# Kernel optimization log

Hardware: AMD Instinct MI355X
Metric: run time of the kernel (lower is better)

The kernel has to match this reference:

```python
import jax, jax.numpy as jnp
import numpy as np

DIM = 1024
STATE = 64
HEADS = 8
EXPAND = 2
INNER = DIM * EXPAND          # 2048
HEAD_DIM = INNER // HEADS     # 256
KERNEL = 4
B, L = 2, 2048
EPS = 1e-5


def setup_inputs() -> dict:
    key = jax.random.key(0)
    ks = jax.random.split(key, 12)
    s = 0.02
    return {
        "input_tensor": jax.random.normal(ks[0], (B, L, DIM), jnp.float32),
        "Wx": jax.random.normal(ks[1], (INNER, DIM), jnp.float32) * s,
        "Wz": jax.random.normal(ks[2], (INNER, DIM), jnp.float32) * s,
        "conv_w": jax.random.normal(ks[3], (INNER, 1, KERNEL), jnp.float32) * s,
        "conv_b": jnp.zeros((INNER,), jnp.float32),
        "Wb": jax.random.normal(ks[4], (HEADS * STATE, INNER), jnp.float32) * s,
        "Wc": jax.random.normal(ks[5], (HEADS * STATE, INNER), jnp.float32) * s,
        "Wdt": jax.random.normal(ks[6], (HEADS, INNER), jnp.float32) * s,
        "b_dt": jnp.zeros((HEADS,), jnp.float32),
        "log_a": jnp.log(jnp.full((HEADS,), 0.5, jnp.float32)),
        "d_param": jnp.ones((HEADS,), jnp.float32),
        "gn_w": jnp.ones((INNER,), jnp.float32),
        "gn_b": jnp.zeros((INNER,), jnp.float32),
        "Wout": jax.random.normal(ks[7], (DIM, INNER), jnp.float32) * s,
    }


def _causal_conv(x, conv_w, conv_b):
    # x: (B, L, INNER); depthwise conv, kernel 4, left-pad 3 (causal)
    x_pad = jnp.pad(x, ((0, 0), (KERNEL - 1, 0), (0, 0)))
    w = conv_w[:, 0, :]  # (INNER, K)
    y = sum(x_pad[:, k:k + x.shape[1], :] * w[:, k] for k in range(KERNEL))
    return y + conv_b


def _ssd_scan(x, b, c, dt, a):
    # x: (B,L,H,P) b,c: (B,L,H,N) dt: (B,L,H) a: (H,)
    state0 = jnp.zeros((x.shape[0], HEADS, STATE, HEAD_DIM), x.dtype)

    def step(state, inp):
        x_t, b_t, c_t, dt_t = inp  # (B,H,P),(B,H,N),(B,H,N),(B,H)
        decay = jnp.exp(dt_t * a)[..., None, None]          # (B,H,1,1)
        b_bar = (dt_t[..., None] * b_t)                      # (B,H,N)
        state = decay * state + b_bar[..., None] * x_t[:, :, None, :]
        y_t = jnp.einsum("bhn,bhnp->bhp", c_t, state)
        return state, y_t

    xs = (x.transpose(1, 0, 2, 3), b.transpose(1, 0, 2, 3),
          c.transpose(1, 0, 2, 3), dt.transpose(1, 0, 2))
    _, ys = jax.lax.scan(step, state0, xs)  # ys: (L,B,H,P)
    return ys.transpose(1, 0, 2, 3)


def reference(input_tensor, Wx, Wz, conv_w, conv_b, Wb, Wc, Wdt, b_dt,
              log_a, d_param, gn_w, gn_b, Wout):
    bsz, seq, _ = input_tensor.shape
    x = input_tensor @ Wx.T               # (B,L,INNER)
    z = input_tensor @ Wz.T
    x = _causal_conv(x, conv_w, conv_b)
    x = jax.nn.silu(x)
    b = (x @ Wb.T).reshape(bsz, seq, HEADS, STATE)
    c = (x @ Wc.T).reshape(bsz, seq, HEADS, STATE)
    dt = jax.nn.softplus(x @ Wdt.T + b_dt)  # (B,L,H)
    xh = x.reshape(bsz, seq, HEADS, HEAD_DIM)
    a = -jnp.exp(log_a)
    y = _ssd_scan(xh, b, c, dt, a)
    y = y + d_param[None, None, :, None] * xh
    # GroupNorm(HEADS, INNER) applied on (B, C, L): normalize per (batch, group)
    # over (channels-in-group, sequence)
    yg = y  # (B, L, H, P) -- groups are contiguous channel blocks = heads
    mean = yg.mean(axis=(1, 3), keepdims=True)
    var = yg.var(axis=(1, 3), keepdims=True)
    yn = (yg - mean) / jnp.sqrt(var + EPS)
    yn = yn * gn_w.reshape(1, 1, HEADS, HEAD_DIM) + gn_b.reshape(1, 1, HEADS, HEAD_DIM)
    yn = yn.reshape(bsz, seq, INNER)
    out = yn * jax.nn.silu(z)
    return out @ Wout.T
```

## Files before the change

### kernel.cpp

```cpp
#include <hip/hip_runtime.h>
#include <math.h>

#define DIM_   1024
#define STATE_ 64
#define HEADS_ 8
#define INNER_ 2048
#define HDIM_  256
#define B_     2
#define L_     2048
#define M_     (B_*L_)
#define EPS_   1e-5f
#define Q_     64
#define NC_    (L_/Q_)
#define NCHUNK_ (B_*HEADS_*NC_)
#define BCS_   1024
#define XZS_   4096

typedef _Float16 f16;
typedef __attribute__((ext_vector_type(8))) _Float16 half8;
typedef __attribute__((ext_vector_type(4))) _Float16 half4;
typedef __attribute__((ext_vector_type(4))) float    f32x4;

__device__ __forceinline__ float siluf(float x) { return x / (1.f + expf(-x)); }

__device__ __forceinline__ void gload_lds16(const void* g, void* l) {
    __builtin_amdgcn_global_load_lds((const __attribute__((address_space(1))) void*)g,
                                     (__attribute__((address_space(3))) void*)l, 16, 0, 0);
}

__global__ __launch_bounds__(256) void cast_all(const float* __restrict__ in0,
                                                const float* __restrict__ Wx,
                                                const float* __restrict__ Wz,
                                                const float* __restrict__ Wb,
                                                const float* __restrict__ Wc,
                                                const float* __restrict__ Wout,
                                                f16* __restrict__ input_h,
                                                f16* __restrict__ wxz_h,
                                                f16* __restrict__ wbc_h,
                                                f16* __restrict__ wout_h) {
    int i = blockIdx.x * 256 + threadIdx.x;
    const float* src; f16* dst; int off;
    if      (i < 1048576) { src = in0;  dst = input_h;            off = i; }
    else if (i < 1572864) { src = Wx;   dst = wxz_h;              off = i - 1048576; }
    else if (i < 2097152) { src = Wz;   dst = wxz_h + 2097152;    off = i - 1572864; }
    else if (i < 2359296) { src = Wb;   dst = wbc_h;              off = i - 2097152; }
    else if (i < 2621440) { src = Wc;   dst = wbc_h + 1048576;    off = i - 2359296; }
    else                  { src = Wout; dst = wout_h;             off = i - 2621440; }
    float4 v = *(const float4*)&src[(size_t)off * 4];
    half4 o;
    o[0] = (f16)v.x; o[1] = (f16)v.y; o[2] = (f16)v.z; o[3] = (f16)v.w;
    *(half4*)&dst[(size_t)off * 4] = o;
}

template<int BN, bool OUTF16>
__global__ __launch_bounds__(256) void hgemm(const f16* __restrict__ A,
                                             const f16* __restrict__ W,
                                             void* __restrict__ Cout,
                                             int K, int N) {
    constexpr int N_FR = BN / 32;
    constexpr int NITER = (128 + BN) / 64;
    __shared__ f16 sA[128 * 32];
    __shared__ f16 sW[BN * 32];
    const int tid  = threadIdx.x;
    const int wid  = tid >> 6;
    const int lane = tid & 63;
    const int bm = blockIdx.y * 128;
    const int bn = blockIdx.x * BN;
    const int wr = wid >> 1, wc = wid & 1;
    const int r  = lane & 15, kg = lane >> 4;

    const f16* gsrc[NITER];
    f16* ldst[NITER];
#pragma unroll
    for (int i = 0; i < NITER; ++i) {
        int slot = tid + i * 256;
        if (slot < 512) {
            int row = slot >> 2;
            int kgv = ((slot & 3) ^ ((row >> 1) & 3)) * 8;
            gsrc[i] = A + (size_t)(bm + row) * K + kgv;
        } else {
            int row = (slot - 512) >> 2;
            int kgv = ((slot & 3) ^ ((row >> 1) & 3)) * 8;
            gsrc[i] = W + (size_t)(bn + row) * K + kgv;
        }
        int slot0 = (tid & ~63) + i * 256;
        ldst[i] = (slot0 < 512) ? &sA[slot0 * 8] : &sW[(slot0 - 512) * 8];
    }

    int aoff[4], boff[N_FR];
#pragma unroll
    for (int m = 0; m < 4; ++m) {
        int arow = wr * 64 + m * 16 + r;
        aoff[m] = arow * 32 + ((kg ^ ((arow >> 1) & 3)) << 3);
    }
#pragma unroll
    for (int n = 0; n < N_FR; ++n) {
        int wrow = wc * (BN / 2) + n * 16 + r;
        boff[n] = wrow * 32 + ((kg ^ ((wrow >> 1) & 3)) << 3);
    }

    f32x4 acc[4][N_FR];
#pragma unroll
    for (int m = 0; m < 4; ++m)
#pragma unroll
        for (int n = 0; n < N_FR; ++n) acc[m][n] = (f32x4)0.f;

    for (int k0 = 0; k0 < K; k0 += 32) {
#pragma unroll
        for (int i = 0; i < NITER; ++i) gload_lds16(gsrc[i] + k0, ldst[i]);
        __syncthreads();
        half8 av[4], bv[N_FR];
#pragma unroll
        for (int m = 0; m < 4; ++m) av[m] = *(const half8*)&sA[aoff[m]];
#pragma unroll
        for (int n = 0; n < N_FR; ++n) bv[n] = *(const half8*)&sW[boff[n]];
#pragma unroll
        for (int m = 0; m < 4; ++m)
#pragma unroll
            for (int n = 0; n < N_FR; ++n)
                acc[m][n] = __builtin_amdgcn_mfma_f32_16x16x32_f16(av[m], bv[n], acc[m][n], 0, 0, 0);
        __syncthreads();
    }

#pragma unroll
    for (int m = 0; m < 4; ++m)
#pragma unroll
        for (int n = 0; n < N_FR; ++n) {
            int row0o = bm + wr * 64 + m * 16 + kg * 4;
            int col   = bn + wc * (BN / 2) + n * 16 + r;
#pragma unroll
            for (int j = 0; j < 4; ++j) {
                if (OUTF16) ((f16*)Cout)[(size_t)(row0o + j) * N + col] = (f16)acc[m][n][j];
                else        ((float*)Cout)[(size_t)(row0o + j) * N + col] = acc[m][n][j];
            }
        }
}

__global__ __launch_bounds__(256) void conv_silu_dt(const f16* __restrict__ xz,
                                                    const float* __restrict__ cw,
                                                    const float* __restrict__ cb,
                                                    const float* __restrict__ Wdt,
                                                    const float* __restrict__ bdt,
                                                    f16* __restrict__ xc,
                                                    float* __restrict__ dtb) {
    __shared__ float sred[4][HEADS_];
    const int m = blockIdx.x;
    const int tid = threadIdx.x;
    const int c8 = tid * 8;
    const int t = m & (L_ - 1);
    float acc[8];
    float4 wv[8];
#pragma unroll
    for (int j = 0; j < 8; ++j) { acc[j] = cb[c8 + j]; wv[j] = *(const float4*)&cw[(c8 + j) * 4]; }
#pragma unroll
    for (int k = 0; k < 4; ++k) {
        int tt = t - 3 + k;
        if (tt >= 0) {
            half8 xv = *(const half8*)&xz[(size_t)(m - 3 + k) * XZS_ + c8];
#pragma unroll
            for (int j = 0; j < 8; ++j) acc[j] += (float)xv[j] * ((const float*)&wv[j])[k];
        }
    }
    float xf[8];
    half8 o;
#pragma unroll
    for (int j = 0; j < 8; ++j) { xf[j] = siluf(acc[j]); o[j] = (f16)xf[j]; }
    *(half8*)&xc[(size_t)m * INNER_ + c8] = o;

    float p[HEADS_];
#pragma unroll
    for (int h = 0; h < HEADS_; ++h) {
        float4 w0 = *(const float4*)&Wdt[h * INNER_ + c8];
        float4 w1 = *(const float4*)&Wdt[h * INNER_ + c8 + 4];
        p[h] = xf[0]*w0.x + xf[1]*w0.y + xf[2]*w0.z + xf[3]*w0.w
             + xf[4]*w1.x + xf[5]*w1.y + xf[6]*w1.z + xf[7]*w1.w;
    }
#pragma unroll
    for (int h = 0; h < HEADS_; ++h)
#pragma unroll
        for (int off = 32; off > 0; off >>= 1)
            p[h] += __shfl_down(p[h], off, 64);
    if ((tid & 63) == 0) {
#pragma unroll
        for (int h = 0; h < HEADS_; ++h) sred[tid >> 6][h] = p[h];
    }
    __syncthreads();
    if (tid < 32) {
        float v = sred[tid >> 3][tid & 7];
        v += __shfl_down(v, 16, 32);
        v += __shfl_down(v, 8, 32);
        if (tid < 8) {
            float s = v + bdt[tid];
            dtb[(size_t)m * HEADS_ + tid] = (s > 20.f) ? s : log1pf(expf(s));
        }
    }
}

__global__ __launch_bounds__(256) void xpose_k(const f16* __restrict__ xc,
                                               f16* __restrict__ xT) {
    __shared__ f16 sT[64][72];
    const int blk = blockIdx.x;
    const int bh = blk >> 7;
    const int rem = blk & 127;
    const int tt = rem >> 2;
    const int pt = rem & 3;
    const int b = bh >> 3, h = bh & 7;
    const int tid = threadIdx.x;
#pragma unroll
    for (int it = 0; it < 2; ++it) {
        int q = tid + it * 256;
        int tr = q >> 3;
        int p0 = (q & 7) * 8;
        half8 v = *(const half8*)&xc[(size_t)(b * L_ + tt * 64 + tr) * INNER_ + h * HDIM_ + pt * 64 + p0];
        *(half8*)&sT[tr][p0] = v;
    }
    __syncthreads();
#pragma unroll
    for (int it = 0; it < 2; ++it) {
        int q = tid + it * 256;
        int pr = q >> 3;
        int t0 = (q & 7) * 8;
        half8 v;
#pragma unroll
        for (int j = 0; j < 8; ++j) v[j] = sT[t0 + j][pr];
        *(half8*)&xT[((size_t)bh * HDIM_ + pt * 64 + pr) * L_ + tt * 64 + t0] = v;
    }
}

__global__ __launch_bounds__(256) void ssd_phase1(const f16* __restrict__ bc,
                                                  const float* __restrict__ dtb,
                                                  const float* __restrict__ log_a,
                                                  f16* __restrict__ pbuf,
                                                  float* __restrict__ eAbuf,
                                                  float* __restrict__ wbuf,
                                                  float* __restrict__ cdecay) {
    __shared__ float sA[Q_];
    __shared__ float sDt[Q_];
    const int tid = threadIdx.x;
    const int chunk = blockIdx.x;
    const int bh = chunk / NC_;
    const int ck = chunk - bh * NC_;
    const int b = bh >> 3, h = bh & 7;
    const int m0 = b * L_ + ck * Q_;

    if (tid < 64) {
        float dt = dtb[(size_t)(m0 + tid) * HEADS_ + h];
        float a = -expf(log_a[h]);
        float x = dt * a;
#pragma unroll
        for (int off = 1; off < 64; off <<= 1) {
            float v = __shfl_up(x, off, 64);
            if (tid >= off) x += v;
        }
        float Alast = __shfl(x, 63, 64);
        sA[tid] = x;
        sDt[tid] = dt;
        eAbuf[(size_t)(m0 + tid) * HEADS_ + h] = expf(x);
        wbuf[(size_t)chunk * Q_ + tid] = expf(Alast - x) * dt;
        if (tid == 0) cdecay[chunk] = expf(Alast);
    }
    __syncthreads();

    const int w = tid >> 6, lane = tid & 63;
    const int r = lane & 15, kg = lane >> 4;
    const int ft = w;
    const f16* Crow = bc + (size_t)(m0 + ft * 16 + r) * BCS_ + 512 + h * STATE_;
    half8 a0 = *(const half8*)(Crow + kg * 8);
    half8 a1 = *(const half8*)(Crow + 32 + kg * 8);
#pragma unroll
    for (int fs = 0; fs < 4; ++fs) {
        const f16* Brow = bc + (size_t)(m0 + fs * 16 + r) * BCS_ + h * STATE_;
        half8 b0 = *(const half8*)(Brow + kg * 8);
        half8 b1 = *(const half8*)(Brow + 32 + kg * 8);
        f32x4 g = (f32x4)0.f;
        g = __builtin_amdgcn_mfma_f32_16x16x32_f16(a0, b0, g, 0, 0, 0);
        g = __builtin_amdgcn_mfma_f32_16x16x32_f16(a1, b1, g, 0, 0, 0);
        int s = fs * 16 + r;
        float As = sA[s], dts = sDt[s];
#pragma unroll
        for (int j = 0; j < 4; ++j) {
            int t = ft * 16 + kg * 4 + j;
            float val = (t >= s) ? g[j] * expf(sA[t] - As) * dts : 0.f;
            pbuf[((size_t)chunk * Q_ + t) * Q_ + s] = (f16)val;
        }
    }
}

__global__ __launch_bounds__(256) void bwt_k(const f16* __restrict__ bc,
                                             const float* __restrict__ wbuf,
                                             f16* __restrict__ bwT) {
    __shared__ f16 sT[64][72];
    __shared__ float sw[64];
    const int chunk = blockIdx.x;
    const int bh = chunk / NC_;
    const int ck = chunk - bh * NC_;
    const int b = bh >> 3, h = bh & 7;
    const int m0 = b * L_ + ck * Q_;
    const int tid = threadIdx.x;
    if (tid < 64) sw[tid] = wbuf[(size_t)chunk * Q_ + tid];
#pragma unroll
    for (int it = 0; it < 2; ++it) {
        int q = tid + it * 256;
        int s = q >> 3;
        int n0 = (q & 7) * 8;
        half8 v = *(const half8*)&bc[(size_t)(m0 + s) * BCS_ + h * STATE_ + n0];
        *(half8*)&sT[s][n0] = v;
    }
    __syncthreads();
#pragma unroll
    for (int it = 0; it < 2; ++it) {
        int q = tid + it * 256;
        int n = q >> 3;
        int s0 = (q & 7) * 8;
        half8 o;
#pragma unroll
        for (int j = 0; j < 8; ++j) o[j] = (f16)((float)sT[s0 + j][n] * sw[s0 + j]);
        *(half8*)&bwT[((size_t)chunk * Q_ + n) * Q_ + s0] = o;
    }
}

__global__ __launch_bounds__(256) void ssd_phase2(const f16* __restrict__ xT,
                                                  const f16* __restrict__ bwT,
                                                  f16* __restrict__ sloc) {
    const int tid = threadIdx.x;
    const int chunk = blockIdx.x;
    const int bh = chunk / NC_;
    const int ck = chunk - bh * NC_;
    const int w = tid >> 6, lane = tid & 63;
    const int r = lane & 15, kg = lane >> 4;

    f32x4 acc[4][4];
#pragma unroll
    for (int i = 0; i < 4; ++i)
#pragma unroll
        for (int j = 0; j < 4; ++j) acc[i][j] = (f32x4)0.f;

#pragma unroll
    for (int kk = 0; kk < 2; ++kk) {
        half8 a[4], bfr[4];
#pragma unroll
        for (int pf = 0; pf < 4; ++pf) {
            int p = w * 64 + pf * 16 + r;
            a[pf] = *(const half8*)&xT[((size_t)bh * HDIM_ + p) * L_ + ck * Q_ + kk * 32 + kg * 8];
        }
#pragma unroll
        for (int nf = 0; nf < 4; ++nf) {
            int n = nf * 16 + r;
            bfr[nf] = *(const half8*)&bwT[((size_t)chunk * Q_ + n) * Q_ + kk * 32 + kg * 8];
        }
#pragma unroll
        for (int pf = 0; pf < 4; ++pf)
#pragma unroll
            for (int nf = 0; nf < 4; ++nf)
                acc[pf][nf] = __builtin_amdgcn_mfma_f32_16x16x32_f16(a[pf], bfr[nf], acc[pf][nf], 0, 0, 0);
    }
#pragma unroll
    for (int pf = 0; pf < 4; ++pf)
#pragma unroll
        for (int nf = 0; nf < 4; ++nf) {
            int n = nf * 16 + r;
#pragma unroll
            for (int j = 0; j < 4; ++j) {
                int p = w * 64 + pf * 16 + kg * 4 + j;
                sloc[((size_t)chunk * HDIM_ + p) * STATE_ + n] = (f16)acc[pf][nf][j];
            }
        }
}

__global__ __launch_bounds__(256) void chunk_scan_k(f16* __restrict__ sloc,
                                                    const float* __restrict__ cdecay) {
    int bh = blockIdx.x >> 6;
    int el = (blockIdx.x & 63) * 256 + threadIdx.x;
    float s = 0.f;
    for (int c = 0; c < NC_; ++c) {
        size_t chunk = (size_t)bh * NC_ + c;
        f16* ptr = sloc + chunk * (size_t)(STATE_*HDIM_) + el;
        float tmp = (float)*ptr;
        *ptr = (f16)s;
        s = cdecay[chunk] * s + tmp;
    }
}

__global__ __launch_bounds__(256) void ssd_phase3(const f16* __restrict__ bc,
                                                  const f16* __restrict__ pbuf,
                                                  const f16* __restrict__ xT,
                                                  const f16* __restrict__ sloc,
                                                  const f16* __restrict__ xch,
                                                  const float* __restrict__ eAbuf,
                                                  const float* __restrict__ dparam,
                                                  f16* __restrict__ ybuf,
                                                  float* __restrict__ gstats) {
    __shared__ float red[512];
    const int tid = threadIdx.x;
    const int chunk = blockIdx.x;
    const int bh = chunk / NC_;
    const int ck = chunk - bh * NC_;
    const int b = bh >> 3, h = bh & 7;
    const int m0 = b * L_ + ck * Q_;
    const int w = tid >> 6, lane = tid & 63;
    const int r = lane & 15, kg = lane >> 4;

    float eA[4];
#pragma unroll
    for (int ft = 0; ft < 4; ++ft)
        eA[ft] = eAbuf[(size_t)(m0 + ft * 16 + r) * HEADS_ + h];

    f32x4 acc[4][4];
#pragma unroll
    for (int i = 0; i < 4; ++i)
#pragma unroll
        for (int j = 0; j < 4; ++j) acc[i][j] = (f32x4)0.f;

#pragma unroll
    for (int ks = 0; ks < 4; ++ks) {
        half8 a[4], bfr[4];
#pragma unroll
        for (int ft = 0; ft < 4; ++ft) {
            int t = ft * 16 + r;
            if (ks < 2) {
                a[ft] = *(const half8*)&pbuf[((size_t)chunk * Q_ + t) * Q_ + ks * 32 + kg * 8];
            } else {
                half8 c = *(const half8*)&bc[(size_t)(m0 + t) * BCS_ + 512 + h * STATE_ + (ks - 2) * 32 + kg * 8];
                half8 sc;
#pragma unroll
                for (int j = 0; j < 8; ++j) sc[j] = (f16)(eA[ft] * (float)c[j]);
                a[ft] = sc;
            }
        }
#pragma unroll
        for (int pf = 0; pf < 4; ++pf) {
            int p = w * 64 + pf * 16 + r;
            if (ks < 2)
                bfr[pf] = *(const half8*)&xT[((size_t)bh * HDIM_ + p) * L_ + ck * Q_ + ks * 32 + kg * 8];
            else
                bfr[pf] = *(const half8*)&sloc[((size_t)chunk * HDIM_ + p) * STATE_ + (ks - 2) * 32 + kg * 8];
        }
#pragma unroll
        for (int ft = 0; ft < 4; ++ft)
#pragma unroll
            for (int pf = 0; pf < 4; ++pf)
                acc[ft][pf] = __builtin_amdgcn_mfma_f32_16x16x32_f16(a[ft], bfr[pf], acc[ft][pf], 0, 0, 0);
    }

    const float d = dparam[h];
    float lsum = 0.f, lsq = 0.f;
#pragma unroll
    for (int ft = 0; ft < 4; ++ft)
#pragma unroll
        for (int pf = 0; pf < 4; ++pf) {
            int p = w * 64 + pf * 16 + r;
#pragma unroll
            for (int j = 0; j < 4; ++j) {
                int t = ft * 16 + kg * 4 + j;
                size_t off = (size_t)(m0 + t) * INNER_ + h * HDIM_ + p;
                float y = acc[ft][pf][j] + d * (float)xch[off];
                ybuf[off] = (f16)y;
                lsum += y; lsq += y * y;
            }
        }
    __syncthreads();
    red[tid] = lsum; red[256 + tid] = lsq;
    __syncthreads();
    for (int st = 128; st > 0; st >>= 1) {
        if (tid < st) { red[tid] += red[tid + st]; red[256 + tid] += red[256 + tid + st]; }
        __syncthreads();
    }
    if (tid == 0) {
        atomicAdd(&gstats[bh * 2 + 0], red[0]);
        atomicAdd(&gstats[bh * 2 + 1], red[256]);
    }
}

__global__ __launch_bounds__(256) void gn_gate_h(const f16* __restrict__ ybuf,
                                                 const f16* __restrict__ xz,
                                                 const float* __restrict__ gstats,
                                                 const float* __restrict__ gnw,
                                                 const float* __restrict__ gnb,
                                                 f16* __restrict__ g) {
    int idx = blockIdx.x * 256 + threadIdx.x;
    int c8 = (idx & (INNER_/8 - 1)) * 8;
    int m = idx >> 8;
    int bh = (m >> 11) * HEADS_ + (c8 >> 8);
    const float cnt = (float)(L_ * HDIM_);
    float mean = gstats[bh*2] / cnt;
    float var  = gstats[bh*2+1] / cnt - mean*mean;
    float rstd = rsqrtf(var + EPS_);
    size_t off = (size_t)m * INNER_ + c8;
    half8 yv = *(const half8*)&ybuf[off];
    half8 zv = *(const half8*)&xz[(size_t)m * XZS_ + INNER_ + c8];
    float4 w0 = *(const float4*)&gnw[c8], w1 = *(const float4*)&gnw[c8+4];
    float4 b0 = *(const float4*)&gnb[c8], b1 = *(const float4*)&gnb[c8+4];
    float wv[8] = {w0.x, w0.y, w0.z, w0.w, w1.x, w1.y, w1.z, w1.w};
    float bv[8] = {b0.x, b0.y, b0.z, b0.w, b1.x, b1.y, b1.z, b1.w};
    half8 o;
#pragma unroll
    for (int j = 0; j < 8; ++j) {
        float v = ((float)yv[j] - mean) * rstd * wv[j] + bv[j];
        o[j] = (f16)(v * siluf((float)zv[j]));
    }
    *(half8*)&g[off] = o;
}

extern "C" void kernel_launch(void* const* d_in, const int* in_sizes, int n_in,
                              void* d_out, int out_size, void* d_ws, size_t ws_size,
                              hipStream_t stream) {
    const float* input  = (const float*)d_in[0];
    const float* Wx     = (const float*)d_in[1];
    const float* Wz     = (const float*)d_in[2];
    const float* conv_w = (const float*)d_in[3];
    const float* conv_b = (const float*)d_in[4];
    const float* Wb     = (const float*)d_in[5];
    const float* Wc     = (const float*)d_in[6];
    const float* Wdt    = (const float*)d_in[7];
    const float* b_dt   = (const float*)d_in[8];
    const float* log_a  = (const float*)d_in[9];
    const float* d_par  = (const float*)d_in[10];
    const float* gn_w   = (const float*)d_in[11];
    const float* gn_b   = (const float*)d_in[12];
    const float* Wout   = (const float*)d_in[13];
    float* out = (float*)d_out;

    float* ws = (float*)d_ws;
    size_t off = 0;
    auto alloc = [&](size_t nfloats) { float* p = ws + off; off += (nfloats + 63) & ~(size_t)63; return p; };
    f16* input_h = (f16*)alloc((size_t)M_*DIM_/2);
    f16* wxz_h   = (f16*)alloc((size_t)XZS_*DIM_/2);
    f16* wbc_h   = (f16*)alloc((size_t)BCS_*INNER_/2);
    f16* wout_h  = (f16*)alloc((size_t)DIM_*INNER_/2);
    f16* xz_h    = (f16*)alloc((size_t)M_*XZS_/2);
    f16* xconv_h = (f16*)alloc((size_t)M_*INNER_/2);
    f16* xT_h    = (f16*)alloc((size_t)M_*INNER_/2);
    f16* gbuf_h  = (f16*)alloc((size_t)M_*INNER_/2);
    f16* bcmat_h = (f16*)alloc((size_t)M_*BCS_/2);
    f16* pbuf_h  = (f16*)alloc((size_t)NCHUNK_*Q_*Q_/2);
    f16* bwT_h   = (f16*)alloc((size_t)NCHUNK_*Q_*Q_/2);
    f16* sloc_h  = (f16*)alloc((size_t)NCHUNK_*STATE_*HDIM_/2);
    f16* ybuf_h  = (f16*)alloc((size_t)M_*INNER_/2);
    float* dtb   = alloc((size_t)M_*HEADS_);
    float* eAb   = alloc((size_t)M_*HEADS_);
    float* wbuf  = alloc((size_t)NCHUNK_*Q_);
    float* cdec  = alloc((size_t)NCHUNK_);
    float* gstat = alloc((size_t)2*B_*HEADS_);

    dim3 blk(256);

    cast_all<<<12288, blk, 0, stream>>>(input, Wx, Wz, Wb, Wc, Wout,
                                        input_h, wxz_h, wbc_h, wout_h);
    hgemm<128,true><<<dim3(XZS_/128, M_/128), blk, 0, stream>>>(input_h, wxz_h, xz_h, DIM_, XZS_);
    conv_silu_dt<<<M_, blk, 0, stream>>>(xz_h, conv_w, conv_b, Wdt, b_dt, xconv_h, dtb);
    hgemm<64,true><<<dim3(BCS_/64, M_/128), blk, 0, stream>>>(xconv_h, wbc_h, bcmat_h, INNER_, BCS_);
    xpose_k<<<2048, blk, 0, stream>>>(xconv_h, xT_h);
    ssd_phase1<<<NCHUNK_, blk, 0, stream>>>(bcmat_h, dtb, log_a, pbuf_h, eAb, wbuf, cdec);
    bwt_k<<<NCHUNK_, blk, 0, stream>>>(bcmat_h, wbuf, bwT_h);
    ssd_phase2<<<NCHUNK_, blk, 0, stream>>>(xT_h, bwT_h, sloc_h);
    chunk_scan_k<<<B_*HEADS_*64, blk, 0, stream>>>(sloc_h, cdec);
    hipMemsetAsync(gstat, 0, 2*B_*HEADS_*sizeof(float), stream);
    ssd_phase3<<<NCHUNK_, blk, 0, stream>>>(bcmat_h, pbuf_h, xT_h, sloc_h, xconv_h,
                                            eAb, d_par, ybuf_h, gstat);
    gn_gate_h<<<(M_*(INNER_/8))/256, blk, 0, stream>>>(ybuf_h, xz_h, gstat, gn_w, gn_b, gbuf_h);
    hgemm<64,false><<<dim3(DIM_/64, M_/128), blk, 0, stream>>>(gbuf_h, wout_h, out, INNER_, DIM_);
}
```

Before: 363.3 us.

## Fuse SSD phases, groupnorm-gate into out GEMM, silu into xz GEMM

Merges ssd_phase1, bwt_k and ssd_phase2 into one kernel that keeps the dt-weighted B matrix in swizzled LDS instead of round-tripping through global memory. Applies silu to z in the xz GEMM epilogue and folds the groupnorm+gate into the A-tile load of the output GEMM, which removes the gbuf intermediate. It also vectorises chunk_scan to 4 elements per thread and replaces the memset by zeroing inside xpose_k. The cost is redundant normalisation work per N-tile in the output GEMM, plus fp16-cast gn weights and a fused A path that is not async.

```diff
diff --git a/kernel.cpp b/kernel.cpp
--- a/kernel.cpp
+++ b/kernel.cpp
@@ -34,10 +34,14 @@
                                                 const float* __restrict__ Wb,
                                                 const float* __restrict__ Wc,
                                                 const float* __restrict__ Wout,
+                                                const float* __restrict__ gw,
+                                                const float* __restrict__ gb,
                                                 f16* __restrict__ input_h,
                                                 f16* __restrict__ wxz_h,
                                                 f16* __restrict__ wbc_h,
-                                                f16* __restrict__ wout_h) {
+                                                f16* __restrict__ wout_h,
+                                                f16* __restrict__ gnw_h,
+                                                f16* __restrict__ gnb_h) {
     int i = blockIdx.x * 256 + threadIdx.x;
     const float* src; f16* dst; int off;
     if      (i < 1048576) { src = in0;  dst = input_h;            off = i; }
@@ -45,14 +49,16 @@
     else if (i < 2097152) { src = Wz;   dst = wxz_h + 2097152;    off = i - 1572864; }
     else if (i < 2359296) { src = Wb;   dst = wbc_h;              off = i - 2097152; }
     else if (i < 2621440) { src = Wc;   dst = wbc_h + 1048576;    off = i - 2359296; }
-    else                  { src = Wout; dst = wout_h;             off = i - 2621440; }
+    else if (i < 3145728) { src = Wout; dst = wout_h;             off = i - 2621440; }
+    else if (i < 3146240) { src = gw;   dst = gnw_h;              off = i - 3145728; }
+    else                  { src = gb;   dst = gnb_h;              off = i - 3146240; }
     float4 v = *(const float4*)&src[(size_t)off * 4];
     half4 o;
     o[0] = (f16)v.x; o[1] = (f16)v.y; o[2] = (f16)v.z; o[3] = (f16)v.w;
     *(half4*)&dst[(size_t)off * 4] = o;
 }
 
-template<int BN, bool OUTF16>
+template<int BN, bool OUTF16, bool SILUZ>
 __global__ __launch_bounds__(256) void hgemm(const f16* __restrict__ A,
                                              const f16* __restrict__ W,
                                              void* __restrict__ Cout,
@@ -130,8 +136,10 @@
             int col   = bn + wc * (BN / 2) + n * 16 + r;
 #pragma unroll
             for (int j = 0; j < 4; ++j) {
-                if (OUTF16) ((f16*)Cout)[(size_t)(row0o + j) * N + col] = (f16)acc[m][n][j];
-                else        ((float*)Cout)[(size_t)(row0o + j) * N + col] = acc[m][n][j];
+                float v = acc[m][n][j];
+                if (SILUZ && col >= INNER_) v = siluf(v);
+                if (OUTF16) ((f16*)Cout)[(size_t)(row0o + j) * N + col] = (f16)v;
+                else        ((float*)Cout)[(size_t)(row0o + j) * N + col] = v;
             }
         }
 }
@@ -197,7 +205,8 @@
 }
 
 __global__ __launch_bounds__(256) void xpose_k(const f16* __restrict__ xc,
-                                               f16* __restrict__ xT) {
+                                               f16* __restrict__ xT,
+                                               float* __restrict__ gstat) {
     __shared__ f16 sT[64][72];
     const int blk = blockIdx.x;
     const int bh = blk >> 7;
@@ -206,6 +215,7 @@
     const int pt = rem & 3;
     const int b = bh >> 3, h = bh & 7;
     const int tid = threadIdx.x;
+    if (blk == 0 && tid < 2 * B_ * HEADS_) gstat[tid] = 0.f;
 #pragma unroll
     for (int it = 0; it < 2; ++it) {
         int q = tid + it * 256;
@@ -227,15 +237,16 @@
     }
 }
 
-__global__ __launch_bounds__(256) void ssd_phase1(const f16* __restrict__ bc,
-                                                  const float* __restrict__ dtb,
-                                                  const float* __restrict__ log_a,
-                                                  f16* __restrict__ pbuf,
-                                                  float* __restrict__ eAbuf,
-                                                  float* __restrict__ wbuf,
-                                                  float* __restrict__ cdecay) {
-    __shared__ float sA[Q_];
-    __shared__ float sDt[Q_];
+__global__ __launch_bounds__(256) void ssd12(const f16* __restrict__ bc,
+                                             const float* __restrict__ dtb,
+                                             const float* __restrict__ log_a,
+                                             const f16* __restrict__ xT,
+                                             f16* __restrict__ pbuf,
+                                             f16* __restrict__ sloc,
+                                             float* __restrict__ eAbuf,
+                                             float* __restrict__ cdecay) {
+    __shared__ float sA[Q_], sDt[Q_], sw[Q_];
+    __shared__ f16 sB[Q_ * Q_];
     const int tid = threadIdx.x;
     const int chunk = blockIdx.x;
     const int bh = chunk / NC_;
@@ -243,6 +254,11 @@
     const int b = bh >> 3, h = bh & 7;
     const int m0 = b * L_ + ck * Q_;
 
+    const int s0 = tid >> 3,        n00 = (tid & 7) * 8;
+    const int s1 = (tid + 256) >> 3, n01 = (tid & 7) * 8;
+    half8 bv0 = *(const half8*)&bc[(size_t)(m0 + s0) * BCS_ + h * STATE_ + n00];
+    half8 bv1 = *(const half8*)&bc[(size_t)(m0 + s1) * BCS_ + h * STATE_ + n01];
+
     if (tid < 64) {
         float dt = dtb[(size_t)(m0 + tid) * HEADS_ + h];
         float a = -expf(log_a[h]);
@@ -255,79 +271,48 @@
         float Alast = __shfl(x, 63, 64);
         sA[tid] = x;
         sDt[tid] = dt;
+        sw[tid] = expf(Alast - x) * dt;
         eAbuf[(size_t)(m0 + tid) * HEADS_ + h] = expf(x);
-        wbuf[(size_t)chunk * Q_ + tid] = expf(Alast - x) * dt;
         if (tid == 0) cdecay[chunk] = expf(Alast);
     }
     __syncthreads();
+
+    {
+        float w0 = sw[s0], w1 = sw[s1];
+        half8 o0, o1;
+#pragma unroll
+        for (int j = 0; j < 8; ++j) { o0[j] = (f16)((float)bv0[j] * w0); o1[j] = (f16)((float)bv1[j] * w1); }
+        *(half8*)&sB[s0 * Q_ + (n00 ^ ((s0 & 7) << 3))] = o0;
+        *(half8*)&sB[s1 * Q_ + (n01 ^ ((s1 & 7) << 3))] = o1;
+    }
 
     const int w = tid >> 6, lane = tid & 63;
     const int r = lane & 15, kg = lane >> 4;
-    const int ft = w;
-    const f16* Crow = bc + (size_t)(m0 + ft * 16 + r) * BCS_ + 512 + h * STATE_;
-    half8 a0 = *(const half8*)(Crow + kg * 8);
-    half8 a1 = *(const half8*)(Crow + 32 + kg * 8);
-#pragma unroll
-    for (int fs = 0; fs < 4; ++fs) {
-        const f16* Brow = bc + (size_t)(m0 + fs * 16 + r) * BCS_ + h * STATE_;
-        half8 b0 = *(const half8*)(Brow + kg * 8);
-        half8 b1 = *(const half8*)(Brow + 32 + kg * 8);
-        f32x4 g = (f32x4)0.f;
-        g = __builtin_amdgcn_mfma_f32_16x16x32_f16(a0, b0, g, 0, 0, 0);
-        g = __builtin_amdgcn_mfma_f32_16x16x32_f16(a1, b1, g, 0, 0, 0);
-        int s = fs * 16 + r;
-        float As = sA[s], dts = sDt[s];
-#pragma unroll
-        for (int j = 0; j < 4; ++j) {
-            int t = ft * 16 + kg * 4 + j;
-            float val = (t >= s) ? g[j] * expf(sA[t] - As) * dts : 0.f;
-            pbuf[((size_t)chunk * Q_ + t) * Q_ + s] = (f16)val;
-        }
-    }
-}
-
-__global__ __launch_bounds__(256) void bwt_k(const f16* __restrict__ bc,
-                                             const float* __restrict__ wbuf,
-                                             f16* __restrict__ bwT) {
-    __shared__ f16 sT[64][72];
-    __shared__ float sw[64];
-    const int chunk = blockIdx.x;
-    const int bh = chunk / NC_;
-    const int ck = chunk - bh * NC_;
-    const int b = bh >> 3, h = bh & 7;
-    const int m0 = b * L_ + ck * Q_;
-    const int tid = threadIdx.x;
-    if (tid < 64) sw[tid] = wbuf[(size_t)chunk * Q_ + tid];
-#pragma unroll
-    for (int it = 0; it < 2; ++it) {
-        int q = tid + it * 256;
-        int s = q >> 3;
-        int n0 = (q & 7) * 8;
-        half8 v = *(const half8*)&bc[(size_t)(m0 + s) * BCS_ + h * STATE_ + n0];
-        *(half8*)&sT[s][n0] = v;
+
+    {
+        const int ft = w;
+        const f16* Crow = bc + (size_t)(m0 + ft * 16 + r) * BCS_ + 512 + h * STATE_;
+        half8 a0 = *(const half8*)(Crow + kg * 8);
+        half8 a1 = *(const half8*)(Crow + 32 + kg * 8);
+#pragma unroll
+        for (int fs = 0; fs < 4; ++fs) {
+            const f16* Brow = bc + (size_t)(m0 + fs * 16 + r) * BCS_ + h * STATE_;
+            half8 b0 = *(const half8*)(Brow + kg * 8);
+            half8 b1 = *(const half8*)(Brow + 32 + kg * 8);
+            f32x4 g = (f32x4)0.f;
+            g = __builtin_amdgcn_mfma_f32_16x16x32_f16(a0, b0, g, 0, 0, 0);
+            g = __builtin_amdgcn_mfma_f32_16x16x32_f16(a1, b1, g, 0, 0, 0);
+            int s = fs * 16 + r;
+            float As = sA[s], dts = sDt[s];
+#pragma unroll
+            for (int j = 0; j < 4; ++j) {
+                int t = ft * 16 + kg * 4 + j;
+                float val = (t >= s) ? g[j] * expf(sA[t] - As) * dts : 0.f;
+                pbuf[((size_t)chunk * Q_ + t) * Q_ + s] = (f16)val;
+            }
+        }
     }
     __syncthreads();
-#pragma unroll
-    for (int it = 0; it < 2; ++it) {
-        int q = tid + it * 256;
-        int n = q >> 3;
-        int s0 = (q & 7) * 8;
-        half8 o;
-#pragma unroll
-        for (int j = 0; j < 8; ++j) o[j] = (f16)((float)sT[s0 + j][n] * sw[s0 + j]);
-        *(half8*)&bwT[((size_t)chunk * Q_ + n) * Q_ + s0] = o;
-    }
-}
-
-__global__ __launch_bounds__(256) void ssd_phase2(const f16* __restrict__ xT,
-                                                  const f16* __restrict__ bwT,
-                                                  f16* __restrict__ sloc) {
-    const int tid = threadIdx.x;
-    const int chunk = blockIdx.x;
-    const int bh = chunk / NC_;
-    const int ck = chunk - bh * NC_;
-    const int w = tid >> 6, lane = tid & 63;
-    const int r = lane & 15, kg = lane >> 4;
 
     f32x4 acc[4][4];
 #pragma unroll
@@ -346,7 +331,13 @@
 #pragma unroll
         for (int nf = 0; nf < 4; ++nf) {
             int n = nf * 16 + r;
-            bfr[nf] = *(const half8*)&bwT[((size_t)chunk * Q_ + n) * Q_ + kk * 32 + kg * 8];
+            half8 v;
+#pragma unroll
+            for (int j = 0; j < 8; ++j) {
+                int s = kk * 32 + kg * 8 + j;
+                v[j] = sB[s * Q_ + (n ^ (j << 3))];
+            }
+            bfr[nf] = v;
         }
 #pragma unroll
         for (int pf = 0; pf < 4; ++pf)
@@ -369,15 +360,20 @@
 
 __global__ __launch_bounds__(256) void chunk_scan_k(f16* __restrict__ sloc,
                                                     const float* __restrict__ cdecay) {
-    int bh = blockIdx.x >> 6;
-    int el = (blockIdx.x & 63) * 256 + threadIdx.x;
-    float s = 0.f;
+    int bh = blockIdx.x >> 4;
+    int el4 = (((blockIdx.x & 15) * 256 + threadIdx.x) << 2);
+    float s0 = 0.f, s1 = 0.f, s2 = 0.f, s3 = 0.f;
     for (int c = 0; c < NC_; ++c) {
         size_t chunk = (size_t)bh * NC_ + c;
-        f16* ptr = sloc + chunk * (size_t)(STATE_*HDIM_) + el;
-        float tmp = (float)*ptr;
-        *ptr = (f16)s;
-        s = cdecay[chunk] * s + tmp;
+        f16* ptr = sloc + chunk * (size_t)(STATE_ * HDIM_) + el4;
+        half4 v = *(const half4*)ptr;
+        half4 o; o[0] = (f16)s0; o[1] = (f16)s1; o[2] = (f16)s2; o[3] = (f16)s3;
+        *(half4*)ptr = o;
+        float d = cdecay[chunk];
+        s0 = d * s0 + (float)v[0];
+        s1 = d * s1 + (float)v[1];
+        s2 = d * s2 + (float)v[2];
+        s3 = d * s3 + (float)v[3];
     }
 }
 
@@ -471,34 +467,115 @@
     }
 }
 
-__global__ __launch_bounds__(256) void gn_gate_h(const f16* __restrict__ ybuf,
-                                                 const f16* __restrict__ xz,
-                                                 const float* __restrict__ gstats,
-                                                 const float* __restrict__ gnw,
-                                                 const float* __restrict__ gnb,
-                                                 f16* __restrict__ g) {
-    int idx = blockIdx.x * 256 + threadIdx.x;
-    int c8 = (idx & (INNER_/8 - 1)) * 8;
-    int m = idx >> 8;
-    int bh = (m >> 11) * HEADS_ + (c8 >> 8);
-    const float cnt = (float)(L_ * HDIM_);
-    float mean = gstats[bh*2] / cnt;
-    float var  = gstats[bh*2+1] / cnt - mean*mean;
-    float rstd = rsqrtf(var + EPS_);
-    size_t off = (size_t)m * INNER_ + c8;
-    half8 yv = *(const half8*)&ybuf[off];
-    half8 zv = *(const half8*)&xz[(size_t)m * XZS_ + INNER_ + c8];
-    float4 w0 = *(const float4*)&gnw[c8], w1 = *(const float4*)&gnw[c8+4];
-    float4 b0 = *(const float4*)&gnb[c8], b1 = *(const float4*)&gnb[c8+4];
-    float wv[8] = {w0.x, w0.y, w0.z, w0.w, w1.x, w1.y, w1.z, w1.w};
-    float bv[8] = {b0.x, b0.y, b0.z, b0.w, b1.x, b1.y, b1.z, b1.w};
-    half8 o;
-#pragma unroll
-    for (int j = 0; j < 8; ++j) {
-        float v = ((float)yv[j] - mean) * rstd * wv[j] + bv[j];
-        o[j] = (f16)(v * siluf((float)zv[j]));
-    }
-    *(half8*)&g[off] = o;
+__global__ __launch_bounds__(256) void hgemm_gate(const f16* __restrict__ ybuf,
+                                                  const f16* __restrict__ xz,
+                                                  const f16* __restrict__ W,
+                                                  const float* __restrict__ gstats,
+                                                  const f16* __restrict__ gnw,
+                                                  const f16* __restrict__ gnb,
+                                                  float* __restrict__ Cout) {
+    constexpr int BN = 64;
+    const int K = INNER_, N = DIM_;
+    __shared__ f16 sA[128 * 32];
+    __shared__ f16 sW[BN * 32];
+    const int tid  = threadIdx.x;
+    const int wid  = tid >> 6;
+    const int lane = tid & 63;
+    const int bm = blockIdx.y * 128;
+    const int bn = blockIdx.x * BN;
+    const int wr = wid >> 1, wc = wid & 1;
+    const int r  = lane & 15, kg = lane >> 4;
+    const float INV_CNT = 1.f / ((float)L_ * HDIM_);
+
+    const int wrow = tid >> 2;
+    const int wkgv = (((tid + 512) & 3) ^ ((wrow >> 1) & 3)) * 8;
+    const f16* gW = W + (size_t)(bn + wrow >= 0 ? bn + wrow : 0) * K + wkgv;
+    f16* lW = &sW[(tid & ~63) * 8];
+
+    int aoff[4], boff[2];
+#pragma unroll
+    for (int m = 0; m < 4; ++m) {
+        int arow = wr * 64 + m * 16 + r;
+        aoff[m] = arow * 32 + ((kg ^ ((arow >> 1) & 3)) << 3);
+    }
+#pragma unroll
+    for (int n = 0; n < 2; ++n) {
+        int wrw = wc * 32 + n * 16 + r;
+        boff[n] = wrw * 32 + ((kg ^ ((wrw >> 1) & 3)) << 3);
+    }
+
+    int srow[2], skgv[2], sm[2];
+#pragma unroll
+    for (int i = 0; i < 2; ++i) {
+        int slot = tid + i * 256;
+        srow[i] = slot >> 2;
+        skgv[i] = ((slot & 3) ^ ((srow[i] >> 1) & 3)) * 8;
+        sm[i] = bm + srow[i];
+    }
+
+    half8 pyv[2], psz[2], pgw[2], pgb[2];
+    auto loadA = [&](int k0) {
+#pragma unroll
+        for (int i = 0; i < 2; ++i) {
+            int c = k0 + skgv[i];
+            pyv[i] = *(const half8*)&ybuf[(size_t)sm[i] * INNER_ + c];
+            psz[i] = *(const half8*)&xz[(size_t)sm[i] * XZS_ + INNER_ + c];
+            pgw[i] = *(const half8*)&gnw[c];
+            pgb[i] = *(const half8*)&gnb[c];
+        }
+    };
+    loadA(0);
+
+    f32x4 acc[4][2];
+#pragma unroll
+    for (int m = 0; m < 4; ++m)
+#pragma unroll
+        for (int n = 0; n < 2; ++n) acc[m][n] = (f32x4)0.f;
+
+    for (int k0 = 0; k0 < K; k0 += 32) {
+        gload_lds16(gW + k0, lW);
+#pragma unroll
+        for (int i = 0; i < 2; ++i) {
+            int c = k0 + skgv[i];
+            int bhid = ((sm[i] >> 11) << 3) + (c >> 8);
+            float mean = gstats[bhid * 2] * INV_CNT;
+            float var  = gstats[bhid * 2 + 1] * INV_CNT - mean * mean;
+            float rstd = rsqrtf(var + EPS_);
+            half8 o;
+#pragma unroll
+            for (int j = 0; j < 8; ++j) {
+                float Aj = rstd * (float)pgw[i][j];
+                float Cj = (float)pgb[i][j] - mean * Aj;
+                float v  = (float)pyv[i][j] * Aj + Cj;
+                o[j] = (f16)(v * (float)psz[i][j]);
+            }
+            *(half8*)&sA[(tid + i * 256) * 8] = o;
+        }
+        if (k0 + 32 < K) loadA(k0 + 32);
+        __syncthreads();
+        half8 av[4], bv[2];
+#pragma unroll
+        for (int m = 0; m < 4; ++m) av[m] = *(const half8*)&sA[aoff[m]];
+#pragma unroll
+        for (int n = 0; n < 2; ++n) bv[n] = *(const half8*)&sW[boff[n]];
+#pragma unroll
+        for (int m = 0; m < 4; ++m)
+#pragma unroll
+            for (int n = 0; n < 2; ++n)
+                acc[m][n] = __builtin_amdgcn_mfma_f32_16x16x32_f16(av[m], bv[n], acc[m][n], 0, 0, 0);
+        __syncthreads();
+    }
+
+#pragma unroll
+    for (int m = 0; m < 4; ++m)
+#pragma unroll
+        for (int n = 0; n < 2; ++n) {
+            int row0o = bm + wr * 64 + m * 16 + kg * 4;
+            int col   = bn + wc * 32 + n * 16 + r;
+#pragma unroll
+            for (int j = 0; j < 4; ++j)
+                Cout[(size_t)(row0o + j) * N + col] = acc[m][n][j];
+        }
 }
 
 extern "C" void kernel_launch(void* const* d_in, const int* in_sizes, int n_in,
@@ -527,36 +604,32 @@
     f16* wxz_h   = (f16*)alloc((size_t)XZS_*DIM_/2);
     f16* wbc_h   = (f16*)alloc((size_t)BCS_*INNER_/2);
     f16* wout_h  = (f16*)alloc((size_t)DIM_*INNER_/2);
+    f16* gnw_h   = (f16*)alloc((size_t)INNER_/2);
+    f16* gnb_h   = (f16*)alloc((size_t)INNER_/2);
     f16* xz_h    = (f16*)alloc((size_t)M_*XZS_/2);
     f16* xconv_h = (f16*)alloc((size_t)M_*INNER_/2);
     f16* xT_h    = (f16*)alloc((size_t)M_*INNER_/2);
-    f16* gbuf_h  = (f16*)alloc((size_t)M_*INNER_/2);
     f16* bcmat_h = (f16*)alloc((size_t)M_*BCS_/2);
     f16* pbuf_h  = (f16*)alloc((size_t)NCHUNK_*Q_*Q_/2);
-    f16* bwT_h   = (f16*)alloc((size_t)NCHUNK_*Q_*Q_/2);
     f16* sloc_h  = (f16*)alloc((size_t)NCHUNK_*STATE_*HDIM_/2);
     f16* ybuf_h  = (f16*)alloc((size_t)M_*INNER_/2);
     float* dtb   = alloc((size_t)M_*HEADS_);
     float* eAb   = alloc((size_t)M_*HEADS_);
-    float* wbuf  = alloc((size_t)NCHUNK_*Q_);
     float* cdec  = alloc((size_t)NCHUNK_);
     float* gstat = alloc((size_t)2*B_*HEADS_);
 
     dim3 blk(256);
 
-    cast_all<<<12288, blk, 0, stream>>>(input, Wx, Wz, Wb, Wc, Wout,
-                                        input_h, wxz_h, wbc_h, wout_h);
-    hgemm<128,true><<<dim3(XZS_/128, M_/128), blk, 0, stream>>>(input_h, wxz_h, xz_h, DIM_, XZS_);
+    cast_all<<<12292, blk, 0, stream>>>(input, Wx, Wz, Wb, Wc, Wout, gn_w, gn_b,
+                                        input_h, wxz_h, wbc_h, wout_h, gnw_h, gnb_h);
+    hgemm<128,true,true><<<dim3(XZS_/128, M_/128), blk, 0, stream>>>(input_h, wxz_h, xz_h, DIM_, XZS_);
     conv_silu_dt<<<M_, blk, 0, stream>>>(xz_h, conv_w, conv_b, Wdt, b_dt, xconv_h, dtb);
-    hgemm<64,true><<<dim3(BCS_/64, M_/128), blk, 0, stream>>>(xconv_h, wbc_h, bcmat_h, INNER_, BCS_);
-    xpose_k<<<2048, blk, 0, stream>>>(xconv_h, xT_h);
-    ssd_phase1<<<NCHUNK_, blk, 0, stream>>>(bcmat_h, dtb, log_a, pbuf_h, eAb, wbuf, cdec);
-    bwt_k<<<NCHUNK_, blk, 0, stream>>>(bcmat_h, wbuf, bwT_h);
-    ssd_phase2<<<NCHUNK_, blk, 0, stream>>>(xT_h, bwT_h, sloc_h);
-    chunk_scan_k<<<B_*HEADS_*64, blk, 0, stream>>>(sloc_h, cdec);
-    hipMemsetAsync(gstat, 0, 2*B_*HEADS_*sizeof(float), stream);
+    hgemm<64,true,false><<<dim3(BCS_/64, M_/128), blk, 0, stream>>>(xconv_h, wbc_h, bcmat_h, INNER_, BCS_);
+    xpose_k<<<2048, blk, 0, stream>>>(xconv_h, xT_h, gstat);
+    ssd12<<<NCHUNK_, blk, 0, stream>>>(bcmat_h, dtb, log_a, xT_h, pbuf_h, sloc_h, eAb, cdec);
+    chunk_scan_k<<<256, blk, 0, stream>>>(sloc_h, cdec);
     ssd_phase3<<<NCHUNK_, blk, 0, stream>>>(bcmat_h, pbuf_h, xT_h, sloc_h, xconv_h,
                                             eAb, d_par, ybuf_h, gstat);
-    gn_gate_h<<<(M_*(INNER_/8))/256, blk, 0, stream>>>(ybuf_h, xz_h, gstat, gn_w, gn_b, gbuf_h);
-    hgemm<64,false><<<dim3(DIM_/64, M_/128), blk, 0, stream>>>(gbuf_h, wout_h, out, INNER_, DIM_);
-}
+    hgemm_gate<<<dim3(DIM_/64, M_/128), blk, 0, stream>>>(ybuf_h, xz_h, wout_h, gstat,
+                                                          gnw_h, gnb_h, out);
+}
```

Measured after the change: 383.8 us. 5.7% more time.

## Fuse SSD phase1/bwt/phase2, remap GEMM blocks across XCDs, vectorize chunk scan

Applied to the files above, without the earlier changes.

Merges ssd_phase1, bwt_k and ssd_phase2 into one kernel that builds the decay-weighted B tile in swizzled shared memory, so the bwT and wbuf buffers are no longer written to and read back from global memory. The GEMM workgroup ids are remapped so neighbouring tiles land on the same XCD, which should improve L2 reuse. The z-gate SiLU moves into the xz GEMM epilogue, the gstat memset is folded into xpose_k, and chunk_scan now handles four elements per thread. The in-kernel gstat zeroing relies on xpose_k finishing before ssd_phase3, which stream order guarantees. The shared-memory gather in the fused kernel reads elements one at a time, which may cost more LDS instructions.

```diff
diff --git a/kernel.cpp b/kernel.cpp
--- a/kernel.cpp
+++ b/kernel.cpp
@@ -52,7 +52,7 @@
     *(half4*)&dst[(size_t)off * 4] = o;
 }
 
-template<int BN, bool OUTF16>
+template<int BN, bool OUTF16, bool SILUZ>
 __global__ __launch_bounds__(256) void hgemm(const f16* __restrict__ A,
                                              const f16* __restrict__ W,
                                              void* __restrict__ Cout,
@@ -64,8 +64,15 @@
     const int tid  = threadIdx.x;
     const int wid  = tid >> 6;
     const int lane = tid & 63;
-    const int bm = blockIdx.y * 128;
-    const int bn = blockIdx.x * BN;
+
+    const int nwg = gridDim.x * gridDim.y;
+    const int id0 = blockIdx.y * gridDim.x + blockIdx.x;
+    const int cpx = nwg >> 3;
+    const int id  = (id0 & 7) * cpx + (id0 >> 3);
+    const int gxsh = __ffs(gridDim.x) - 1;
+    const int bm = (id >> gxsh) * 128;
+    const int bn = (id & (gridDim.x - 1)) * BN;
+
     const int wr = wid >> 1, wc = wid & 1;
     const int r  = lane & 15, kg = lane >> 4;
 
@@ -130,8 +137,10 @@
             int col   = bn + wc * (BN / 2) + n * 16 + r;
 #pragma unroll
             for (int j = 0; j < 4; ++j) {
-                if (OUTF16) ((f16*)Cout)[(size_t)(row0o + j) * N + col] = (f16)acc[m][n][j];
-                else        ((float*)Cout)[(size_t)(row0o + j) * N + col] = acc[m][n][j];
+                float v = acc[m][n][j];
+                if (SILUZ && col >= INNER_) v = siluf(v);
+                if (OUTF16) ((f16*)Cout)[(size_t)(row0o + j) * N + col] = (f16)v;
+                else        ((float*)Cout)[(size_t)(row0o + j) * N + col] = v;
             }
         }
 }
@@ -197,7 +206,8 @@
 }
 
 __global__ __launch_bounds__(256) void xpose_k(const f16* __restrict__ xc,
-                                               f16* __restrict__ xT) {
+                                               f16* __restrict__ xT,
+                                               float* __restrict__ gstat) {
     __shared__ f16 sT[64][72];
     const int blk = blockIdx.x;
     const int bh = blk >> 7;
@@ -206,6 +216,7 @@
     const int pt = rem & 3;
     const int b = bh >> 3, h = bh & 7;
     const int tid = threadIdx.x;
+    if (blk == 0 && tid < 2 * B_ * HEADS_) gstat[tid] = 0.f;
 #pragma unroll
     for (int it = 0; it < 2; ++it) {
         int q = tid + it * 256;
@@ -227,15 +238,16 @@
     }
 }
 
-__global__ __launch_bounds__(256) void ssd_phase1(const f16* __restrict__ bc,
-                                                  const float* __restrict__ dtb,
-                                                  const float* __restrict__ log_a,
-                                                  f16* __restrict__ pbuf,
-                                                  float* __restrict__ eAbuf,
-                                                  float* __restrict__ wbuf,
-                                                  float* __restrict__ cdecay) {
-    __shared__ float sA[Q_];
-    __shared__ float sDt[Q_];
+__global__ __launch_bounds__(256) void ssd12(const f16* __restrict__ bc,
+                                             const float* __restrict__ dtb,
+                                             const float* __restrict__ log_a,
+                                             const f16* __restrict__ xT,
+                                             f16* __restrict__ pbuf,
+                                             f16* __restrict__ sloc,
+                                             float* __restrict__ eAbuf,
+                                             float* __restrict__ cdecay) {
+    __shared__ float sA[Q_], sDt[Q_], sw[Q_];
+    __shared__ f16 sB[Q_ * Q_];
     const int tid = threadIdx.x;
     const int chunk = blockIdx.x;
     const int bh = chunk / NC_;
@@ -243,6 +255,11 @@
     const int b = bh >> 3, h = bh & 7;
     const int m0 = b * L_ + ck * Q_;
 
+    const int s0 = tid >> 3,        n00 = (tid & 7) * 8;
+    const int s1 = (tid + 256) >> 3, n01 = (tid & 7) * 8;
+    half8 bv0 = *(const half8*)&bc[(size_t)(m0 + s0) * BCS_ + h * STATE_ + n00];
+    half8 bv1 = *(const half8*)&bc[(size_t)(m0 + s1) * BCS_ + h * STATE_ + n01];
+
     if (tid < 64) {
         float dt = dtb[(size_t)(m0 + tid) * HEADS_ + h];
         float a = -expf(log_a[h]);
@@ -255,79 +272,48 @@
         float Alast = __shfl(x, 63, 64);
         sA[tid] = x;
         sDt[tid] = dt;
+        sw[tid] = expf(Alast - x) * dt;
         eAbuf[(size_t)(m0 + tid) * HEADS_ + h] = expf(x);
-        wbuf[(size_t)chunk * Q_ + tid] = expf(Alast - x) * dt;
         if (tid == 0) cdecay[chunk] = expf(Alast);
     }
     __syncthreads();
+
+    {
+        float w0 = sw[s0], w1 = sw[s1];
+        half8 o0, o1;
+#pragma unroll
+        for (int j = 0; j < 8; ++j) { o0[j] = (f16)((float)bv0[j] * w0); o1[j] = (f16)((float)bv1[j] * w1); }
+        *(half8*)&sB[s0 * Q_ + (n00 ^ ((s0 & 7) << 3))] = o0;
+        *(half8*)&sB[s1 * Q_ + (n01 ^ ((s1 & 7) << 3))] = o1;
+    }
 
     const int w = tid >> 6, lane = tid & 63;
     const int r = lane & 15, kg = lane >> 4;
-    const int ft = w;
-    const f16* Crow = bc + (size_t)(m0 + ft * 16 + r) * BCS_ + 512 + h * STATE_;
-    half8 a0 = *(const half8*)(Crow + kg * 8);
-    half8 a1 = *(const half8*)(Crow + 32 + kg * 8);
-#pragma unroll
-    for (int fs = 0; fs < 4; ++fs) {
-        const f16* Brow = bc + (size_t)(m0 + fs * 16 + r) * BCS_ + h * STATE_;
-        half8 b0 = *(const half8*)(Brow + kg * 8);
-        half8 b1 = *(const half8*)(Brow + 32 + kg * 8);
-        f32x4 g = (f32x4)0.f;
-        g = __builtin_amdgcn_mfma_f32_16x16x32_f16(a0, b0, g, 0, 0, 0);
-        g = __builtin_amdgcn_mfma_f32_16x16x32_f16(a1, b1, g, 0, 0, 0);
-        int s = fs * 16 + r;
-        float As = sA[s], dts = sDt[s];
-#pragma unroll
-        for (int j = 0; j < 4; ++j) {
-            int t = ft * 16 + kg * 4 + j;
-            float val = (t >= s) ? g[j] * expf(sA[t] - As) * dts : 0.f;
-            pbuf[((size_t)chunk * Q_ + t) * Q_ + s] = (f16)val;
-        }
-    }
-}
-
-__global__ __launch_bounds__(256) void bwt_k(const f16* __restrict__ bc,
-                                             const float* __restrict__ wbuf,
-                                             f16* __restrict__ bwT) {
-    __shared__ f16 sT[64][72];
-    __shared__ float sw[64];
-    const int chunk = blockIdx.x;
-    const int bh = chunk / NC_;
-    const int ck = chunk - bh * NC_;
-    const int b = bh >> 3, h = bh & 7;
-    const int m0 = b * L_ + ck * Q_;
-    const int tid = threadIdx.x;
-    if (tid < 64) sw[tid] = wbuf[(size_t)chunk * Q_ + tid];
-#pragma unroll
-    for (int it = 0; it < 2; ++it) {
-        int q = tid + it * 256;
-        int s = q >> 3;
-        int n0 = (q & 7) * 8;
-        half8 v = *(const half8*)&bc[(size_t)(m0 + s) * BCS_ + h * STATE_ + n0];
-        *(half8*)&sT[s][n0] = v;
+
+    {
+        const int ft = w;
+        const f16* Crow = bc + (size_t)(m0 + ft * 16 + r) * BCS_ + 512 + h * STATE_;
+        half8 a0 = *(const half8*)(Crow + kg * 8);
+        half8 a1 = *(const half8*)(Crow + 32 + kg * 8);
+#pragma unroll
+        for (int fs = 0; fs < 4; ++fs) {
+            const f16* Brow = bc + (size_t)(m0 + fs * 16 + r) * BCS_ + h * STATE_;
+            half8 b0 = *(const half8*)(Brow + kg * 8);
+            half8 b1 = *(const half8*)(Brow + 32 + kg * 8);
+            f32x4 g = (f32x4)0.f;
+            g = __builtin_amdgcn_mfma_f32_16x16x32_f16(a0, b0, g, 0, 0, 0);
+            g = __builtin_amdgcn_mfma_f32_16x16x32_f16(a1, b1, g, 0, 0, 0);
+            int s = fs * 16 + r;
+            float As = sA[s], dts = sDt[s];
+#pragma unroll
+            for (int j = 0; j < 4; ++j) {
+                int t = ft * 16 + kg * 4 + j;
+                float val = (t >= s) ? g[j] * expf(sA[t] - As) * dts : 0.f;
+                pbuf[((size_t)chunk * Q_ + t) * Q_ + s] = (f16)val;
+            }
+        }
     }
     __syncthreads();
-#pragma unroll
-    for (int it = 0; it < 2; ++it) {
-        int q = tid + it * 256;
-        int n = q >> 3;
-        int s0 = (q & 7) * 8;
-        half8 o;
-#pragma unroll
-        for (int j = 0; j < 8; ++j) o[j] = (f16)((float)sT[s0 + j][n] * sw[s0 + j]);
-        *(half8*)&bwT[((size_t)chunk * Q_ + n) * Q_ + s0] = o;
-    }
-}
-
-__global__ __launch_bounds__(256) void ssd_phase2(const f16* __restrict__ xT,
-                                                  const f16* __restrict__ bwT,
-                                                  f16* __restrict__ sloc) {
-    const int tid = threadIdx.x;
-    const int chunk = blockIdx.x;
-    const int bh = chunk / NC_;
-    const int ck = chunk - bh * NC_;
-    const int w = tid >> 6, lane = tid & 63;
-    const int r = lane & 15, kg = lane >> 4;
 
     f32x4 acc[4][4];
 #pragma unroll
@@ -346,7 +332,13 @@
 #pragma unroll
         for (int nf = 0; nf < 4; ++nf) {
             int n = nf * 16 + r;
-            bfr[nf] = *(const half8*)&bwT[((size_t)chunk * Q_ + n) * Q_ + kk * 32 + kg * 8];
+            half8 v;
+#pragma unroll
+            for (int j = 0; j < 8; ++j) {
+                int s = kk * 32 + kg * 8 + j;
+                v[j] = sB[s * Q_ + (n ^ (j << 3))];
+            }
+            bfr[nf] = v;
         }
 #pragma unroll
         for (int pf = 0; pf < 4; ++pf)
@@ -369,15 +361,20 @@
 
 __global__ __launch_bounds__(256) void chunk_scan_k(f16* __restrict__ sloc,
                                                     const float* __restrict__ cdecay) {
-    int bh = blockIdx.x >> 6;
-    int el = (blockIdx.x & 63) * 256 + threadIdx.x;
-    float s = 0.f;
+    int bh = blockIdx.x >> 4;
+    int el4 = (((blockIdx.x & 15) * 256 + threadIdx.x) << 2);
+    float s0 = 0.f, s1 = 0.f, s2 = 0.f, s3 = 0.f;
     for (int c = 0; c < NC_; ++c) {
         size_t chunk = (size_t)bh * NC_ + c;
-        f16* ptr = sloc + chunk * (size_t)(STATE_*HDIM_) + el;
-        float tmp = (float)*ptr;
-        *ptr = (f16)s;
-        s = cdecay[chunk] * s + tmp;
+        f16* ptr = sloc + chunk * (size_t)(STATE_ * HDIM_) + el4;
+        half4 v = *(const half4*)ptr;
+        half4 o; o[0] = (f16)s0; o[1] = (f16)s1; o[2] = (f16)s2; o[3] = (f16)s3;
+        *(half4*)ptr = o;
+        float d = cdecay[chunk];
+        s0 = d * s0 + (float)v[0];
+        s1 = d * s1 + (float)v[1];
+        s2 = d * s2 + (float)v[2];
+        s3 = d * s3 + (float)v[3];
     }
 }
 
@@ -496,7 +493,7 @@
 #pragma unroll
     for (int j = 0; j < 8; ++j) {
         float v = ((float)yv[j] - mean) * rstd * wv[j] + bv[j];
-        o[j] = (f16)(v * siluf((float)zv[j]));
+        o[j] = (f16)(v * (float)zv[j]);
     }
     *(half8*)&g[off] = o;
 }
@@ -533,12 +530,10 @@
     f16* gbuf_h  = (f16*)alloc((size_t)M_*INNER_/2);
     f16* bcmat_h = (f16*)alloc((size_t)M_*BCS_/2);
     f16* pbuf_h  = (f16*)alloc((size_t)NCHUNK_*Q_*Q_/2);
-    f16* bwT_h   = (f16*)alloc((size_t)NCHUNK_*Q_*Q_/2);
     f16* sloc_h  = (f16*)alloc((size_t)NCHUNK_*STATE_*HDIM_/2);
     f16* ybuf_h  = (f16*)alloc((size_t)M_*INNER_/2);
     float* dtb   = alloc((size_t)M_*HEADS_);
     float* eAb   = alloc((size_t)M_*HEADS_);
-    float* wbuf  = alloc((size_t)NCHUNK_*Q_);
     float* cdec  = alloc((size_t)NCHUNK_);
     float* gstat = alloc((size_t)2*B_*HEADS_);
 
@@ -546,17 +541,14 @@
 
     cast_all<<<12288, blk, 0, stream>>>(input, Wx, Wz, Wb, Wc, Wout,
                                         input_h, wxz_h, wbc_h, wout_h);
-    hgemm<128,true><<<dim3(XZS_/128, M_/128), blk, 0, stream>>>(input_h, wxz_h, xz_h, DIM_, XZS_);
+    hgemm<128,true,true><<<dim3(XZS_/128, M_/128), blk, 0, stream>>>(input_h, wxz_h, xz_h, DIM_, XZS_);
     conv_silu_dt<<<M_, blk, 0, stream>>>(xz_h, conv_w, conv_b, Wdt, b_dt, xconv_h, dtb);
-    hgemm<64,true><<<dim3(BCS_/64, M_/128), blk, 0, stream>>>(xconv_h, wbc_h, bcmat_h, INNER_, BCS_);
-    xpose_k<<<2048, blk, 0, stream>>>(xconv_h, xT_h);
-    ssd_phase1<<<NCHUNK_, blk, 0, stream>>>(bcmat_h, dtb, log_a, pbuf_h, eAb, wbuf, cdec);
-    bwt_k<<<NCHUNK_, blk, 0, stream>>>(bcmat_h, wbuf, bwT_h);
-    ssd_phase2<<<NCHUNK_, blk, 0, stream>>>(xT_h, bwT_h, sloc_h);
-    chunk_scan_k<<<B_*HEADS_*64, blk, 0, stream>>>(sloc_h, cdec);
-    hipMemsetAsync(gstat, 0, 2*B_*HEADS_*sizeof(float), stream);
+    hgemm<64,true,false><<<dim3(BCS_/64, M_/128), blk, 0, stream>>>(xconv_h, wbc_h, bcmat_h, INNER_, BCS_);
+    xpose_k<<<2048, blk, 0, stream>>>(xconv_h, xT_h, gstat);
+    ssd12<<<NCHUNK_, blk, 0, stream>>>(bcmat_h, dtb, log_a, xT_h, pbuf_h, sloc_h, eAb, cdec);
+    chunk_scan_k<<<256, blk, 0, stream>>>(sloc_h, cdec);
     ssd_phase3<<<NCHUNK_, blk, 0, stream>>>(bcmat_h, pbuf_h, xT_h, sloc_h, xconv_h,
                                             eAb, d_par, ybuf_h, gstat);
     gn_gate_h<<<(M_*(INNER_/8))/256, blk, 0, stream>>>(ybuf_h, xz_h, gstat, gn_w, gn_b, gbuf_h);
-    hgemm<64,false><<<dim3(DIM_/64, M_/128), blk, 0, stream>>>(gbuf_h, wout_h, out, INNER_, DIM_);
-}
+    hgemm<64,false,false><<<dim3(DIM_/64, M_/128), blk, 0, stream>>>(gbuf_h, wout_h, out, INNER_, DIM_);
+}
```

After: 363.2 us. About the same (-0.0%).
